# Performance work log

Measured on AMD Instinct MI355X. Metric: run time of the kernel, lower is better.

## Reference

```python
import jax, jax.numpy as jnp
import numpy as np
from jax import lax

B, D, K = 256, 128, 8192


def _conv_same(x, w, b):
    # x: [B,C,H,W], w: [O,I,3,3] (torch Conv2d layout), stride 1, padding 1 == SAME
    y = lax.conv_general_dilated(x, w, (1, 1), 'SAME',
                                 dimension_numbers=('NCHW', 'OIHW', 'NCHW'))
    return y + b[None, :, None, None]


def _convT_same(x, w, b):
    # torch ConvTranspose2d(k=3, stride=1, padding=1) with weight [I,O,3,3]
    # == SAME conv with spatially flipped kernel and swapped in/out channels
    wt = jnp.flip(w, axis=(2, 3)).transpose(1, 0, 2, 3)  # -> [O,I,3,3]
    return _conv_same(x, wt, b)


def setup_inputs() -> dict:
    key = jax.random.key(0)
    ks = jax.random.split(key, 12)
    s = 0.05
    return {
        'patch':  jax.random.normal(ks[0], (B, 3, 64, 64), jnp.float32),
        'enc_w1': jax.random.normal(ks[1], (64, 3, 3, 3), jnp.float32) * s,
        'enc_b1': jnp.zeros((64,), jnp.float32),
        'enc_w2': jax.random.normal(ks[2], (D, 64, 3, 3), jnp.float32) * s,
        'enc_b2': jnp.zeros((D,), jnp.float32),
        'emb':    jax.random.normal(ks[3], (K, D), jnp.float32),
        'dec_w1': jax.random.normal(ks[4], (D, 64, 3, 3), jnp.float32) * s,  # ConvT [in,out,k,k]
        'dec_b1': jnp.zeros((64,), jnp.float32),
        'dec_w2': jax.random.normal(ks[5], (64, 64, 3, 3), jnp.float32) * s,
        'dec_b2': jnp.zeros((64,), jnp.float32),
        'dec_w3': jax.random.normal(ks[6], (64, 3, 3, 3), jnp.float32) * s,
        'dec_b3': jnp.zeros((3,), jnp.float32),
    }


def reference(patch, enc_w1, enc_b1, enc_w2, enc_b2, emb,
              dec_w1, dec_b1, dec_w2, dec_b2, dec_w3, dec_b3):
    # ---- encode_patch ----
    h = jax.nn.relu(_conv_same(patch, enc_w1, enc_b1))
    h = _conv_same(h, enc_w2, enc_b2)
    z = jnp.mean(h, axis=(2, 3))  # AdaptiveAvgPool2d((1,1)) + flatten -> [B,D]

    # ---- VQ: cdist + argmin + gather ----
    # argmin over squared L2 == argmin over cdist(p=2); avoid sqrt.
    d2 = (jnp.sum(z * z, axis=1, keepdims=True)
          + jnp.sum(emb * emb, axis=1)[None, :]
          - 2.0 * z @ emb.T)  # [B,K]
    encoding_indices = jnp.argmin(d2, axis=1)  # [B]
    z_q = emb[encoding_indices]  # [B,D]

    commitment_loss = jnp.mean((lax.stop_gradient(z_q) - z) ** 2)
    codebook_loss = jnp.mean((z_q - lax.stop_gradient(z)) ** 2)

    # ---- decode_vector ----
    # bilinear interpolate of a 1x1 map to 64x64 is a pure broadcast
    v = jnp.broadcast_to(z_q[:, :, None, None], (z_q.shape[0], z_q.shape[1], 64, 64))
    d = jax.nn.relu(_convT_same(v, dec_w1, dec_b1))
    d = jax.nn.relu(_convT_same(d, dec_w2, dec_b2))
    recon = jnp.tanh(_convT_same(d, dec_w3, dec_b3))  # [B,3,64,64]

    return recon, codebook_loss, commitment_loss, encoding_indices[:, None]
```

## Files before the change

### kernel.cpp

```cpp
#include <hip/hip_runtime.h>
#include <math.h>


__global__ __launch_bounds__(256) void k_conv1_pre(
    const float* __restrict__ patch, const float* __restrict__ w1,
    const float* __restrict__ b1, const float* __restrict__ dw1,
    const float* __restrict__ emb, float* __restrict__ pstat,
    float* __restrict__ Wcfg, float* __restrict__ en2)
{
    __shared__ __align__(16) float lds[2304];
    const int blk = blockIdx.x;
    const int tid = threadIdx.x;

    if (blk >= 2048) {
        const int gid = (blk - 2048) * 256 + tid;
        if (gid < 73728) {
            const int cfg = gid >> 13;
            const int o = (gid >> 7) & 63;
            const int i = gid & 127;
            const int cy = cfg / 3, cx = cfg % 3;
            const int ylo = (cy == 2) ? 1 : 0, yhi = (cy == 0) ? 1 : 2;
            const int xlo = (cx == 2) ? 1 : 0, xhi = (cx == 0) ? 1 : 2;
            const float* wp = dw1 + ((size_t)i * 64 + o) * 9;
            float s = 0.f;
            for (int ky = ylo; ky <= yhi; ++ky)
                for (int kx = xlo; kx <= xhi; ++kx)
                    s += wp[ky * 3 + kx];
            Wcfg[gid] = s;
        } else if (gid < 81920) {
            const int k = gid - 73728;
            const float4* e = (const float4*)(emb + (size_t)k * 128);
            float s = 0.f;
            for (int t = 0; t < 32; ++t) {
                float4 v = e[t];
                s = fmaf(v.x, v.x, fmaf(v.y, v.y, fmaf(v.z, v.z, fmaf(v.w, v.w, s))));
            }
            en2[k] = s;
        }
        return;
    }

    const int b = blk >> 3, rg = blk & 7;
    const int y0 = rg * 8;
    const float* pb = patch + (size_t)b * 12288;
    for (int i = tid; i < 2160; i += 256) {
        const int c = i / 720, rem = i - c * 720;
        const int r = rem / 72, p = rem - r * 72;
        const int y = y0 + r - 1, x = p - 3;
        float v = 0.f;
        if (y >= 0 && y < 64 && x >= 0 && x < 64)
            v = pb[(c << 12) + (y << 6) + x];
        lds[i] = v;
    }
    __syncthreads();

    const int ch = tid & 63, q = tid >> 6;
    float w[3][3][3];
#pragma unroll
    for (int ic = 0; ic < 3; ++ic)
#pragma unroll
        for (int ky = 0; ky < 3; ++ky)
#pragma unroll
            for (int kx = 0; kx < 3; ++kx)
                w[ic][ky][kx] = w1[((ch * 3 + ic) * 3 + ky) * 3 + kx];
    const float bias = b1[ch];

    float T = 0, r0s = 0, r63s = 0, c0s = 0, c63s = 0;
    float h00 = 0, h063 = 0, h630 = 0, h6363 = 0;

#pragma unroll
    for (int sub = 0; sub < 2; ++sub) {
        const int yl = q * 2 + sub;
        const bool isr0  = (rg == 0) && (yl == 0);
        const bool isr63 = (rg == 7) && (yl == 7);
        float cr[3][3][2];
#pragma unroll
        for (int ic = 0; ic < 3; ++ic)
#pragma unroll
            for (int ky = 0; ky < 3; ++ky) {
                const float2 t2 = *(const float2*)&lds[(ic * 10 + yl + ky) * 72 + 2];
                cr[ic][ky][0] = t2.x; cr[ic][ky][1] = t2.y;
            }
#pragma unroll 4
        for (int xc = 0; xc < 16; ++xc) {
            float a0 = bias, a1 = bias, a2 = bias, a3 = bias;
#pragma unroll
            for (int ic = 0; ic < 3; ++ic)
#pragma unroll
                for (int ky = 0; ky < 3; ++ky) {
                    const float4 nw = *(const float4*)&lds[(ic * 10 + yl + ky) * 72 + xc * 4 + 4];
                    const float w0 = w[ic][ky][0], w1v = w[ic][ky][1], w2v = w[ic][ky][2];
                    a0 = fmaf(w0, cr[ic][ky][0], fmaf(w1v, cr[ic][ky][1], fmaf(w2v, nw.x, a0)));
                    a1 = fmaf(w0, cr[ic][ky][1], fmaf(w1v, nw.x, fmaf(w2v, nw.y, a1)));
                    a2 = fmaf(w0, nw.x, fmaf(w1v, nw.y, fmaf(w2v, nw.z, a2)));
                    a3 = fmaf(w0, nw.y, fmaf(w1v, nw.z, fmaf(w2v, nw.w, a3)));
                    cr[ic][ky][0] = nw.z; cr[ic][ky][1] = nw.w;
                }
            a0 = fmaxf(a0, 0.f); a1 = fmaxf(a1, 0.f);
            a2 = fmaxf(a2, 0.f); a3 = fmaxf(a3, 0.f);
            const float rs = (a0 + a1) + (a2 + a3);
            T += rs;
            if (isr0)  { r0s += rs;  if (xc == 0) h00 = a0;  if (xc == 15) h063 = a3; }
            if (isr63) { r63s += rs; if (xc == 0) h630 = a0; if (xc == 15) h6363 = a3; }
            if (xc == 0)  c0s += a0;
            if (xc == 15) c63s += a3;
        }
    }
    __syncthreads();
    float st[9] = {T, r0s, r63s, c0s, c63s, h00, h063, h630, h6363};
#pragma unroll
    for (int s = 0; s < 9; ++s) lds[(s * 4 + q) * 64 + ch] = st[s];
    __syncthreads();
    if (tid < 64) {
        float* pp = pstat + (size_t)blk * 576;
#pragma unroll
        for (int s = 0; s < 9; ++s)
            pp[s * 64 + tid] = lds[(s * 4 + 0) * 64 + tid] + lds[(s * 4 + 1) * 64 + tid]
                             + lds[(s * 4 + 2) * 64 + tid] + lds[(s * 4 + 3) * 64 + tid];
    }
}

__global__ __launch_bounds__(256) void k_zred(
    const float* __restrict__ pstat, const float* __restrict__ w2,
    const float* __restrict__ b2, float* __restrict__ z, float* __restrict__ zn2)
{
    __shared__ float fst[576];
    __shared__ __align__(16) float Ssh[576];
    __shared__ float zp[256];
    __shared__ float red2[128];
    const int b = blockIdx.x, tid = threadIdx.x;

    const float* pp = pstat + (size_t)b * 8 * 576;
    for (int i = tid; i < 576; i += 256) {
        float s = 0.f;
#pragma unroll
        for (int g = 0; g < 8; ++g) s += pp[g * 576 + i];
        fst[i] = s;
    }
    __syncthreads();

    if (tid < 64) {
        const int ch = tid;
        const float Tt   = fst[0 * 64 + ch], R0  = fst[1 * 64 + ch], R63 = fst[2 * 64 + ch];
        const float C0   = fst[3 * 64 + ch], C63 = fst[4 * 64 + ch];
        const float H00  = fst[5 * 64 + ch], H063 = fst[6 * 64 + ch];
        const float H630 = fst[7 * 64 + ch], H6363 = fst[8 * 64 + ch];
#pragma unroll
        for (int ky = 0; ky < 3; ++ky) {
            const float rex = (ky == 0) ? R63 : (ky == 2 ? R0 : 0.f);
#pragma unroll
            for (int kx = 0; kx < 3; ++kx) {
                const float cex = (kx == 0) ? C63 : (kx == 2 ? C0 : 0.f);
                float corner = 0.f;
                if (ky == 0 && kx == 0) corner = H6363;
                if (ky == 0 && kx == 2) corner = H630;
                if (ky == 2 && kx == 0) corner = H063;
                if (ky == 2 && kx == 2) corner = H00;
                Ssh[ch * 9 + ky * 3 + kx] = (Tt - rex - cex + corner) * (1.f / 4096.f);
            }
        }
    }
    __syncthreads();

    const int oc = tid & 127, h = tid >> 7;
    const float4* Wv = (const float4*)(w2 + (size_t)oc * 576 + h * 288);
    const float4* Sv = (const float4*)(Ssh + h * 288);
    float acc = 0.f;
    for (int t = 0; t < 72; ++t) {
        const float4 w4 = Wv[t], s4 = Sv[t];
        acc = fmaf(w4.x, s4.x, acc);
        acc = fmaf(w4.y, s4.y, acc);
        acc = fmaf(w4.z, s4.z, acc);
        acc = fmaf(w4.w, s4.w, acc);
    }
    zp[tid] = acc;
    __syncthreads();
    if (tid < 128) {
        const float zv = b2[tid] + zp[tid] + zp[tid + 128];
        z[(size_t)b * 128 + tid] = zv;
        red2[tid] = zv * zv;
    }
    __syncthreads();
    if (tid < 64) {
        float v = red2[tid] + red2[tid + 64];
        v += __shfl_xor(v, 32); v += __shfl_xor(v, 16); v += __shfl_xor(v, 8);
        v += __shfl_xor(v, 4);  v += __shfl_xor(v, 2);  v += __shfl_xor(v, 1);
        if (tid == 0) zn2[b] = v;
    }
}

__global__ __launch_bounds__(256) void k_vq(
    const float* __restrict__ z, const float* __restrict__ emb,
    const float* __restrict__ en2, float* __restrict__ pd2, int* __restrict__ pidx)
{
    __shared__ __align__(16) float zsh[2048];
    __shared__ float wd[16][4];
    __shared__ int   wi[16][4];
    const int tid = threadIdx.x;
    const int bg = blockIdx.x >> 4, kc = blockIdx.x & 15;
    const int b0 = bg * 16;
    for (int i = tid; i < 2048; i += 256) zsh[i] = z[(size_t)b0 * 128 + i];
    __syncthreads();

    const int k0 = kc * 512 + tid, k1 = k0 + 256;
    const float4* e0 = (const float4*)(emb + (size_t)k0 * 128);
    const float4* e1 = (const float4*)(emb + (size_t)k1 * 128);
    const float4* zv = (const float4*)zsh;

    float acc0[16], acc1[16];
#pragma unroll
    for (int bb = 0; bb < 16; ++bb) { acc0[bb] = 0.f; acc1[bb] = 0.f; }

    for (int t = 0; t < 32; ++t) {
        const float4 ea = e0[t], eb = e1[t];
#pragma unroll
        for (int bb = 0; bb < 16; ++bb) {
            const float4 zz = zv[bb * 32 + t];
            acc0[bb] = fmaf(zz.x, ea.x, fmaf(zz.y, ea.y, fmaf(zz.z, ea.z, fmaf(zz.w, ea.w, acc0[bb]))));
            acc1[bb] = fmaf(zz.x, eb.x, fmaf(zz.y, eb.y, fmaf(zz.z, eb.z, fmaf(zz.w, eb.w, acc1[bb]))));
        }
    }
    const float E0 = en2[k0], E1 = en2[k1];
    const int wv_ = tid >> 6, ln = tid & 63;
#pragma unroll
    for (int bb = 0; bb < 16; ++bb) {
        const float da = fmaf(-2.f, acc0[bb], E0);
        const float db = fmaf(-2.f, acc1[bb], E1);
        float d; int ix;
        if (da <= db) { d = da; ix = k0; } else { d = db; ix = k1; }
#pragma unroll
        for (int off = 32; off > 0; off >>= 1) {
            const float od = __shfl_xor(d, off);
            const int   oi = __shfl_xor(ix, off);
            if (od < d || (od == d && oi < ix)) { d = od; ix = oi; }
        }
        if (ln == 0) { wd[bb][wv_] = d; wi[bb][wv_] = ix; }
    }
    __syncthreads();
    if (tid < 16) {
        float d = wd[tid][0]; int ix = wi[tid][0];
#pragma unroll
        for (int wv2 = 1; wv2 < 4; ++wv2) {
            const float od = wd[tid][wv2]; const int oi = wi[tid][wv2];
            if (od < d || (od == d && oi < ix)) { d = od; ix = oi; }
        }
        pd2[(b0 + tid) * 16 + kc] = d;
        pidx[(b0 + tid) * 16 + kc] = ix;
    }
}

__global__ __launch_bounds__(256) void k_decode(
    const float* __restrict__ emb, const float* __restrict__ zn2,
    const float* __restrict__ pd2, const int* __restrict__ pidx,
    const float* __restrict__ Wcfg, const float* __restrict__ db1,
    const float* __restrict__ dw2, const float* __restrict__ db2,
    const float* __restrict__ dw3, const float* __restrict__ db3,
    float* __restrict__ out)
{
    __shared__ __align__(16) float zsh[128];
    __shared__ float d1e[64][10];
    __shared__ float d2e[64][26];
    __shared__ float o3[3 * 49];
    __shared__ int   bisld[256];
    __shared__ float redl[256];

    const int b = blockIdx.x, tid = threadIdx.x;

    float dmin = pd2[tid * 16]; int bi = pidx[tid * 16];
    for (int j = 1; j < 16; ++j) {
        const float d = pd2[tid * 16 + j]; const int ix = pidx[tid * 16 + j];
        if (d < dmin || (d == dmin && ix < bi)) { dmin = d; bi = ix; }
    }
    bisld[tid] = bi;
    redl[tid] = dmin + zn2[tid];
    __syncthreads();

    const int mybi = bisld[b];
    if (tid < 128) { zsh[tid] = emb[(size_t)mybi * 128 + tid]; redl[tid] += redl[tid + 128]; }
    if (tid >= 128 && tid < 192) { d1e[tid - 128][9] = 0.f; d2e[tid - 128][25] = 0.f; }
    __syncthreads();
    if (tid < 64) {
        float v = redl[tid] + redl[tid + 64];
        v += __shfl_xor(v, 32); v += __shfl_xor(v, 16); v += __shfl_xor(v, 8);
        v += __shfl_xor(v, 4);  v += __shfl_xor(v, 2);  v += __shfl_xor(v, 1);
        if (tid == 0 && b == 0) {
            const float L = v * (1.f / 32768.f);
            out[3145728] = L;
            out[3145729] = L;
        }
    }
    if (b == 0) out[3145730 + tid] = (float)bisld[tid];

    for (int id = tid; id < 576; id += 256) {
        const int o = id / 9, cfg = id % 9;
        const float4* wv = (const float4*)(Wcfg + ((size_t)cfg * 64 + o) * 128);
        const float4* zv = (const float4*)zsh;
        float acc = db1[o];
        for (int t = 0; t < 32; ++t) {
            const float4 w4 = wv[t], z4 = zv[t];
            acc = fmaf(w4.x, z4.x, acc);
            acc = fmaf(w4.y, z4.y, acc);
            acc = fmaf(w4.z, z4.z, acc);
            acc = fmaf(w4.w, z4.w, acc);
        }
        d1e[o][cfg] = fmaxf(acc, 0.f);
    }
    __syncthreads();

    {
        const int TY5[5][3] = {{-1,0,1},{0,1,1},{1,1,1},{1,1,2},{1,2,-1}};
        const int o = tid >> 2, isub = tid & 3;
        float acc[25];
#pragma unroll
        for (int c = 0; c < 25; ++c) acc[c] = 0.f;
        for (int ii = 0; ii < 16; ++ii) {
            const int i = isub + ii * 4;
            float d1v[10];
#pragma unroll
            for (int t = 0; t < 9; ++t) d1v[t] = d1e[i][t];
            d1v[9] = 0.f;
            float w9[9];
            const float* wp = dw2 + ((size_t)i * 64 + o) * 9;
#pragma unroll
            for (int t = 0; t < 9; ++t) w9[t] = wp[t];
#pragma unroll
            for (int cy = 0; cy < 5; ++cy) {
#pragma unroll
                for (int ky = 0; ky < 3; ++ky) {
                    const int ty = TY5[cy][ky];
                    if (ty < 0) continue;
#pragma unroll
                    for (int cx = 0; cx < 5; ++cx) {
#pragma unroll
                        for (int kx = 0; kx < 3; ++kx) {
                            const int tx = TY5[cx][kx];
                            if (tx < 0) continue;
                            acc[cy * 5 + cx] = fmaf(w9[(2 - ky) * 3 + (2 - kx)],
                                                    d1v[ty * 3 + tx], acc[cy * 5 + cx]);
                        }
                    }
                }
            }
        }
#pragma unroll
        for (int c = 0; c < 25; ++c) {
            float v = acc[c];
            v += __shfl_xor(v, 1);
            v += __shfl_xor(v, 2);
            if (isub == 0) d2e[o][c] = fmaxf(v + db2[o], 0.f);
        }
    }
    __syncthreads();

    if (tid < 147) {
        const int TY7[7][3] = {{-1,0,1},{0,1,2},{1,2,2},{2,2,2},{2,2,3},{2,3,4},{3,4,-1}};
        const int c3 = tid / 49, cc = tid % 49, cy = cc / 7, cx = cc % 7;
        float acc = db3[c3];
        for (int i = 0; i < 64; ++i) {
            const float* wp = dw3 + ((size_t)i * 3 + c3) * 9;
#pragma unroll
            for (int ky = 0; ky < 3; ++ky) {
                const int ty = TY7[cy][ky];
#pragma unroll
                for (int kx = 0; kx < 3; ++kx) {
                    const int tx = TY7[cx][kx];
                    const int t = (ty < 0 || tx < 0) ? 25 : ty * 5 + tx;
                    acc = fmaf(wp[(2 - ky) * 3 + (2 - kx)], d2e[i][t], acc);
                }
            }
        }
        o3[c3 * 49 + cc] = tanhf(acc);
    }
    __syncthreads();

    float4* ob = (float4*)(out + (size_t)b * 12288);
    for (int id = tid; id < 3072; id += 256) {
        const int base = id * 4;
        const int c = base >> 12, rem = base & 4095, y = rem >> 6, x0 = rem & 63;
        const int ry = (y <= 3) ? y : (y >= 60 ? y - 57 : 3);
        const float* row = &o3[c * 49 + ry * 7];
        float4 v;
        int x;
        x = x0 + 0; v.x = row[(x <= 3) ? x : (x >= 60 ? x - 57 : 3)];
        x = x0 + 1; v.y = row[(x <= 3) ? x : (x >= 60 ? x - 57 : 3)];
        x = x0 + 2; v.z = row[(x <= 3) ? x : (x >= 60 ? x - 57 : 3)];
        x = x0 + 3; v.w = row[(x <= 3) ? x : (x >= 60 ? x - 57 : 3)];
        ob[id] = v;
    }
}

extern "C" void kernel_launch(void* const* d_in, const int* in_sizes, int n_in,
                              void* d_out, int out_size, void* d_ws, size_t ws_size,
                              hipStream_t stream)
{
    const float* patch  = (const float*)d_in[0];
    const float* enc_w1 = (const float*)d_in[1];
    const float* enc_b1 = (const float*)d_in[2];
    const float* enc_w2 = (const float*)d_in[3];
    const float* enc_b2 = (const float*)d_in[4];
    const float* emb    = (const float*)d_in[5];
    const float* dec_w1 = (const float*)d_in[6];
    const float* dec_b1 = (const float*)d_in[7];
    const float* dec_w2 = (const float*)d_in[8];
    const float* dec_b2 = (const float*)d_in[9];
    const float* dec_w3 = (const float*)d_in[10];
    const float* dec_b3 = (const float*)d_in[11];

    float* out = (float*)d_out;
    float* ws  = (float*)d_ws;

    float* pstat = ws;
    float* z     = ws + 1179648;
    float* zn2   = ws + 1212416;
    float* pd2   = ws + 1212672;
    int*   pidx  = (int*)(ws + 1216768);
    float* Wcfg  = ws + 1220864;
    float* en2   = ws + 1294592;

    k_conv1_pre<<<dim3(2368), dim3(256), 0, stream>>>(patch, enc_w1, enc_b1, dec_w1,
                                                      emb, pstat, Wcfg, en2);
    k_zred<<<dim3(256), dim3(256), 0, stream>>>(pstat, enc_w2, enc_b2, z, zn2);
    k_vq<<<dim3(256), dim3(256), 0, stream>>>(z, emb, en2, pd2, pidx);
    k_decode<<<dim3(256), dim3(256), 0, stream>>>(emb, zn2, pd2, pidx, Wcfg, dec_b1,
                                                  dec_w2, dec_b2, dec_w3, dec_b3, out);
}
```

Measured before the change: 131.3 us.

## Halve VQ batch tile, stage decoder weights in LDS, vectorise weight loads

The VQ kernel now handles 8 batch rows per block instead of 16 and launches twice as many blocks (512), so more of the GPU is used during the codebook distance search, though each embedding row is now loaded from memory twice as often. The decoder kernel copies the last-layer weights into shared memory instead of reading them from global memory in its inner loop. It also loads the second-layer weights with unaligned 4-wide vector loads. Finally, it broadcasts the selected index through a single shared variable instead of a 256-entry array, plus some cosmetic reassociation and renames.

```diff
diff --git a/kernel.cpp b/kernel.cpp
--- a/kernel.cpp
+++ b/kernel.cpp
@@ -1,5 +1,7 @@
 #include <hip/hip_runtime.h>
 #include <math.h>
+
+typedef float float4u __attribute__((ext_vector_type(4), aligned(4)));
 
 
 __global__ __launch_bounds__(256) void k_conv1_pre(
@@ -107,16 +109,18 @@
         }
     }
     __syncthreads();
-    float st[9] = {T, r0s, r63s, c0s, c63s, h00, h063, h630, h6363};
-#pragma unroll
-    for (int s = 0; s < 9; ++s) lds[(s * 4 + q) * 64 + ch] = st[s];
+    {
+        const float st[9] = {T, r0s, r63s, c0s, c63s, h00, h063, h630, h6363};
+#pragma unroll
+        for (int s = 0; s < 9; ++s) lds[(s * 4 + q) * 64 + ch] = st[s];
+    }
     __syncthreads();
     if (tid < 64) {
         float* pp = pstat + (size_t)blk * 576;
 #pragma unroll
         for (int s = 0; s < 9; ++s)
-            pp[s * 64 + tid] = lds[(s * 4 + 0) * 64 + tid] + lds[(s * 4 + 1) * 64 + tid]
-                             + lds[(s * 4 + 2) * 64 + tid] + lds[(s * 4 + 3) * 64 + tid];
+            pp[s * 64 + tid] = (lds[(s * 4 + 0) * 64 + tid] + lds[(s * 4 + 1) * 64 + tid])
+                             + (lds[(s * 4 + 2) * 64 + tid] + lds[(s * 4 + 3) * 64 + tid]);
     }
 }
 
@@ -140,11 +144,10 @@
     __syncthreads();
 
     if (tid < 64) {
-        const int ch = tid;
-        const float Tt   = fst[0 * 64 + ch], R0  = fst[1 * 64 + ch], R63 = fst[2 * 64 + ch];
-        const float C0   = fst[3 * 64 + ch], C63 = fst[4 * 64 + ch];
-        const float H00  = fst[5 * 64 + ch], H063 = fst[6 * 64 + ch];
-        const float H630 = fst[7 * 64 + ch], H6363 = fst[8 * 64 + ch];
+        const float Tt   = fst[0 * 64 + tid], R0  = fst[1 * 64 + tid], R63 = fst[2 * 64 + tid];
+        const float C0   = fst[3 * 64 + tid], C63 = fst[4 * 64 + tid];
+        const float H00  = fst[5 * 64 + tid], H063 = fst[6 * 64 + tid];
+        const float H630 = fst[7 * 64 + tid], H6363 = fst[8 * 64 + tid];
 #pragma unroll
         for (int ky = 0; ky < 3; ++ky) {
             const float rex = (ky == 0) ? R63 : (ky == 2 ? R0 : 0.f);
@@ -156,7 +159,7 @@
                 if (ky == 0 && kx == 2) corner = H630;
                 if (ky == 2 && kx == 0) corner = H063;
                 if (ky == 2 && kx == 2) corner = H00;
-                Ssh[ch * 9 + ky * 3 + kx] = (Tt - rex - cex + corner) * (1.f / 4096.f);
+                Ssh[tid * 9 + ky * 3 + kx] = (Tt - rex - cex + corner) * (1.f / 4096.f);
             }
         }
     }
@@ -193,13 +196,13 @@
     const float* __restrict__ z, const float* __restrict__ emb,
     const float* __restrict__ en2, float* __restrict__ pd2, int* __restrict__ pidx)
 {
-    __shared__ __align__(16) float zsh[2048];
-    __shared__ float wd[16][4];
-    __shared__ int   wi[16][4];
+    __shared__ __align__(16) float zsh[1024];
+    __shared__ float wd[8][4];
+    __shared__ int   wi[8][4];
     const int tid = threadIdx.x;
     const int bg = blockIdx.x >> 4, kc = blockIdx.x & 15;
-    const int b0 = bg * 16;
-    for (int i = tid; i < 2048; i += 256) zsh[i] = z[(size_t)b0 * 128 + i];
+    const int b0 = bg * 8;
+    for (int i = tid; i < 1024; i += 256) zsh[i] = z[(size_t)b0 * 128 + i];
     __syncthreads();
 
     const int k0 = kc * 512 + tid, k1 = k0 + 256;
@@ -207,14 +210,14 @@
     const float4* e1 = (const float4*)(emb + (size_t)k1 * 128);
     const float4* zv = (const float4*)zsh;
 
-    float acc0[16], acc1[16];
-#pragma unroll
-    for (int bb = 0; bb < 16; ++bb) { acc0[bb] = 0.f; acc1[bb] = 0.f; }
+    float acc0[8], acc1[8];
+#pragma unroll
+    for (int bb = 0; bb < 8; ++bb) { acc0[bb] = 0.f; acc1[bb] = 0.f; }
 
     for (int t = 0; t < 32; ++t) {
         const float4 ea = e0[t], eb = e1[t];
 #pragma unroll
-        for (int bb = 0; bb < 16; ++bb) {
+        for (int bb = 0; bb < 8; ++bb) {
             const float4 zz = zv[bb * 32 + t];
             acc0[bb] = fmaf(zz.x, ea.x, fmaf(zz.y, ea.y, fmaf(zz.z, ea.z, fmaf(zz.w, ea.w, acc0[bb]))));
             acc1[bb] = fmaf(zz.x, eb.x, fmaf(zz.y, eb.y, fmaf(zz.z, eb.z, fmaf(zz.w, eb.w, acc1[bb]))));
@@ -223,7 +226,7 @@
     const float E0 = en2[k0], E1 = en2[k1];
     const int wv_ = tid >> 6, ln = tid & 63;
 #pragma unroll
-    for (int bb = 0; bb < 16; ++bb) {
+    for (int bb = 0; bb < 8; ++bb) {
         const float da = fmaf(-2.f, acc0[bb], E0);
         const float db = fmaf(-2.f, acc1[bb], E1);
         float d; int ix;
@@ -237,7 +240,7 @@
         if (ln == 0) { wd[bb][wv_] = d; wi[bb][wv_] = ix; }
     }
     __syncthreads();
-    if (tid < 16) {
+    if (tid < 8) {
         float d = wd[tid][0]; int ix = wi[tid][0];
 #pragma unroll
         for (int wv2 = 1; wv2 < 4; ++wv2) {
@@ -261,8 +264,9 @@
     __shared__ float d1e[64][10];
     __shared__ float d2e[64][26];
     __shared__ float o3[3 * 49];
-    __shared__ int   bisld[256];
+    __shared__ float dw3sh[1728];
     __shared__ float redl[256];
+    __shared__ int bsel;
 
     const int b = blockIdx.x, tid = threadIdx.x;
 
@@ -271,14 +275,19 @@
         const float d = pd2[tid * 16 + j]; const int ix = pidx[tid * 16 + j];
         if (d < dmin || (d == dmin && ix < bi)) { dmin = d; bi = ix; }
     }
-    bisld[tid] = bi;
+    if (tid == b) bsel = bi;
     redl[tid] = dmin + zn2[tid];
     __syncthreads();
 
-    const int mybi = bisld[b];
-    if (tid < 128) { zsh[tid] = emb[(size_t)mybi * 128 + tid]; redl[tid] += redl[tid + 128]; }
-    if (tid >= 128 && tid < 192) { d1e[tid - 128][9] = 0.f; d2e[tid - 128][25] = 0.f; }
-    __syncthreads();
+    if (b == 0) out[3145730 + tid] = (float)bi;
+    if (tid < 128) {
+        redl[tid] += redl[tid + 128];
+        zsh[tid] = emb[(size_t)bsel * 128 + tid];
+    }
+    for (int id = tid; id < 1728; id += 256) dw3sh[id] = dw3[id];
+    if (tid < 64) { d1e[tid][9] = 0.f; d2e[tid][25] = 0.f; }
+    __syncthreads();
+
     if (tid < 64) {
         float v = redl[tid] + redl[tid + 64];
         v += __shfl_xor(v, 32); v += __shfl_xor(v, 16); v += __shfl_xor(v, 8);
@@ -289,10 +298,9 @@
             out[3145729] = L;
         }
     }
-    if (b == 0) out[3145730 + tid] = (float)bisld[tid];
 
     for (int id = tid; id < 576; id += 256) {
-        const int o = id / 9, cfg = id % 9;
+        const int o = id / 9, cfg = id - o * 9;
         const float4* wv = (const float4*)(Wcfg + ((size_t)cfg * 64 + o) * 128);
         const float4* zv = (const float4*)zsh;
         float acc = db1[o];
@@ -312,17 +320,18 @@
         const int o = tid >> 2, isub = tid & 3;
         float acc[25];
 #pragma unroll
-        for (int c = 0; c < 25; ++c) acc[c] = 0.f;
+        for (int cc = 0; cc < 25; ++cc) acc[cc] = 0.f;
         for (int ii = 0; ii < 16; ++ii) {
             const int i = isub + ii * 4;
             float d1v[10];
 #pragma unroll
             for (int t = 0; t < 9; ++t) d1v[t] = d1e[i][t];
             d1v[9] = 0.f;
-            float w9[9];
             const float* wp = dw2 + ((size_t)i * 64 + o) * 9;
-#pragma unroll
-            for (int t = 0; t < 9; ++t) w9[t] = wp[t];
+            const float4u w03 = *(const float4u*)wp;
+            const float4u w47 = *(const float4u*)(wp + 4);
+            const float w8v = wp[8];
+            const float w9[9] = {w03.x, w03.y, w03.z, w03.w, w47.x, w47.y, w47.z, w47.w, w8v};
 #pragma unroll
             for (int cy = 0; cy < 5; ++cy) {
 #pragma unroll
@@ -343,11 +352,11 @@
             }
         }
 #pragma unroll
-        for (int c = 0; c < 25; ++c) {
-            float v = acc[c];
+        for (int cc = 0; cc < 25; ++cc) {
+            float v = acc[cc];
             v += __shfl_xor(v, 1);
             v += __shfl_xor(v, 2);
-            if (isub == 0) d2e[o][c] = fmaxf(v + db2[o], 0.f);
+            if (isub == 0) d2e[o][cc] = fmaxf(v + db2[o], 0.f);
         }
     }
     __syncthreads();
@@ -357,7 +366,7 @@
         const int c3 = tid / 49, cc = tid % 49, cy = cc / 7, cx = cc % 7;
         float acc = db3[c3];
         for (int i = 0; i < 64; ++i) {
-            const float* wp = dw3 + ((size_t)i * 3 + c3) * 9;
+            const float* wp = &dw3sh[(i * 3 + c3) * 9];
 #pragma unroll
             for (int ky = 0; ky < 3; ++ky) {
                 const int ty = TY7[cy][ky];
@@ -420,7 +429,7 @@
     k_conv1_pre<<<dim3(2368), dim3(256), 0, stream>>>(patch, enc_w1, enc_b1, dec_w1,
                                                       emb, pstat, Wcfg, en2);
     k_zred<<<dim3(256), dim3(256), 0, stream>>>(pstat, enc_w2, enc_b2, z, zn2);
-    k_vq<<<dim3(256), dim3(256), 0, stream>>>(z, emb, en2, pd2, pidx);
+    k_vq<<<dim3(512), dim3(256), 0, stream>>>(z, emb, en2, pd2, pidx);
     k_decode<<<dim3(256), dim3(256), 0, stream>>>(emb, zn2, pd2, pidx, Wcfg, dec_b1,
                                                   dec_w2, dec_b2, dec_w3, dec_b3, out);
 }
```

New measurement: 134.3 us. +2.3%, slower.
